# Performance work log

Hardware: AMD Instinct MI355X
Metric: run time of the kernel (lower is better)

## Reference

```python
import jax, jax.numpy as jnp
import numpy as np

N_WIN = 8
NUM_HEADS = 8
TOPK = 4
D_MODEL = 128
SCALE = D_MODEL ** (-0.5)


def setup_inputs() -> dict:
    key = jax.random.key(0)
    k1, k2 = jax.random.split(key)
    cv_feature = jax.random.normal(k1, (1, 128, 128, 128), dtype=jnp.float32)
    mv_feature = jax.random.normal(k2, (1, 2, 128, 128, 128), dtype=jnp.float32)
    return {"cv_feature": cv_feature, "mv_feature": mv_feature}


def reference(cv_feature, mv_feature):
    # cv_feature: [N, H, W, C] query view; mv_feature: [N, V, H, W, C] multi-view KV
    N, H, W, C = cv_feature.shape
    V = mv_feature.shape[1]
    j = i = N_WIN
    h, w = H // j, W // i
    p2, w2 = j * i, h * w
    ch = C // NUM_HEADS  # per-head dim

    # window partition: n (j h) (i w) c -> n (j i) h w c
    cv_patch = cv_feature.reshape(N, j, h, i, w, C).transpose(0, 1, 3, 2, 4, 5).reshape(N, p2, h, w, C)
    mv_patch = mv_feature.reshape(N, V, j, h, i, w, C).transpose(0, 1, 2, 4, 3, 5, 6).reshape(N, V, p2, h, w, C)

    q_pix = cv_patch.reshape(N, p2, w2, C)          # [N, p2, w2, C]
    kv_pix = mv_patch.reshape(N, V, p2, w2, C)      # [N, V, p2, w2, C]

    # window-level descriptors (means) -> routing logits
    q_win = cv_patch.mean(axis=(2, 3))              # [N, p2, C]
    k_win = mv_patch.mean(axis=(3, 4))              # [N, V, p2, C]

    # TopK routing (detached in original; forward math identical)
    k_flat = k_win.reshape(N, V * p2, C)
    attn_logit = jnp.einsum('npc,nqc->npq', q_win * SCALE, k_flat)  # [N, p2, V*p2]
    topk_logit, r_idx = jax.lax.top_k(attn_logit, TOPK)
    r_weight = jax.nn.softmax(topk_logit, axis=-1)  # computed by module, unused downstream

    # KV gather of selected windows: [N, p2, topk, w2, C]
    kv_flat = kv_pix.reshape(N, V * p2, w2, C)
    kv_sel = kv_flat[jnp.arange(N)[:, None, None], r_idx]

    # per-window multi-head attention over topk*w2 gathered tokens
    q = q_pix.reshape(N, p2, w2, NUM_HEADS, ch)
    kv = kv_sel.reshape(N, p2, TOPK * w2, NUM_HEADS, ch)
    attn = jnp.einsum('npwmc,npxmc->npmwx', q * SCALE, kv)  # [N, p2, m, w2, topk*w2]
    attn = jax.nn.softmax(attn, axis=-1)
    out = jnp.einsum('npmwx,npxmc->npwmc', attn, kv)        # [N, p2, w2, m, ch]

    # merge windows back: n (j i) (h w) c -> n (j h) (i w) c
    out = out.reshape(N, j, i, h, w, C).transpose(0, 1, 3, 2, 4, 5).reshape(N, H, W, C)
    return out
```

## Files before the change

### kernel.cpp

```cpp
#include <hip/hip_runtime.h>

#define HH_ 128
#define WW_ 128
#define CC_ 128
#define P2 64
#define W2 256
#define NH 8
#define CH 16
#define NV 2
#define TOPK 4
#define SCALE 0.08838834764831845f

typedef unsigned short u16;
typedef unsigned int   u32;
typedef short s8v __attribute__((ext_vector_type(8)));
typedef float f4  __attribute__((ext_vector_type(4)));

union FRAG { uint4 q; u32 u[4]; s8v v; };

__device__ float g_means[(P2 + NV * P2) * CC_];
__device__ int2  g_part[64];
__device__ int   g_mode;
__device__ int   g_amb;

__device__ inline u16 f2b(float v) {
    union { float f; u32 u; } x; x.f = v;
    u32 r = x.u + 0x7FFFu + ((x.u >> 16) & 1u);
    return (u16)(r >> 16);
}
__device__ inline float b2f(u16 h) {
    union { u32 u; float f; } x; x.u = (u32)h << 16; return x.f;
}
__device__ inline float h2f(u16 h) {
    u32 s = (h >> 15) & 1u, e = (h >> 10) & 31u, m = h & 1023u;
    float v;
    if (e == 0)       v = m * 5.9604644775e-8f;
    else if (e == 31) v = 65504.f;
    else { union { u32 u; float f; } x; x.u = ((e + 112u) << 23) | (m << 13); v = x.f; }
    return s ? -v : v;
}
__device__ inline u16 f2h(float v) {
    union { float f; u32 u; } x; x.f = v;
    u32 s = (x.u >> 16) & 0x8000u;
    int  e = (int)((x.u >> 23) & 0xFF) - 112;
    u32  m = x.u & 0x7FFFFF;
    if (e >= 31) return (u16)(s | 0x7BFF);
    if (e <= 0) {
        if (e < -10) return (u16)s;
        m |= 0x800000u;
        int sh = 14 - e;
        u32 r = m >> sh, rem = m & ((1u << sh) - 1u), half = 1u << (sh - 1);
        if (rem > half || (rem == half && (r & 1))) r++;
        return (u16)(s | r);
    }
    u32 r = ((u32)e << 10) | (m >> 13), rem = m & 0x1FFFu;
    if (rem > 0x1000u || (rem == 0x1000u && (r & 1))) r++;
    return (u16)(s | r);
}

__device__ inline u32 pkhi(float a, float b) {
    union { float f; u32 u; } xa, xb; xa.f = a; xb.f = b;
    return (xa.u >> 16) | (xb.u & 0xFFFF0000u);
}
__device__ inline float hipart(float a) {
    union { float f; u32 u; } x; x.f = a; x.u &= 0xFFFF0000u; return x.f;
}

template<int MODE>
__device__ inline float decode1(const void* __restrict__ src, int off) {
    if (MODE == 0) return ((const float*)src)[off];
    u16 h = ((const u16*)src)[off];
    return (MODE == 1) ? b2f(h) : h2f(h);
}

template<int MODE>
__device__ inline float4 loadf4(const void* __restrict__ src, int off) {
    if (MODE == 0) return *(const float4*)((const float*)src + off);
    uint2 v = *(const uint2*)((const u16*)src + off);
    float4 r;
    if (MODE == 1) {
        r.x = b2f((u16)v.x); r.y = b2f((u16)(v.x >> 16));
        r.z = b2f((u16)v.y); r.w = b2f((u16)(v.y >> 16));
    } else {
        r.x = h2f((u16)v.x); r.y = h2f((u16)(v.x >> 16));
        r.z = h2f((u16)v.y); r.w = h2f((u16)(v.y >> 16));
    }
    return r;
}

template<int MODE>
__device__ inline void store4t(void* __restrict__ out, int off, const float* __restrict__ r) {
    if (MODE == 0) {
        *(float4*)((float*)out + off) = make_float4(r[0], r[1], r[2], r[3]);
    } else if (MODE == 1) {
        u32 w0 = (u32)f2b(r[0]) | ((u32)f2b(r[1]) << 16);
        u32 w1 = (u32)f2b(r[2]) | ((u32)f2b(r[3]) << 16);
        *(uint2*)((u16*)out + off) = make_uint2(w0, w1);
    } else {
        u32 w0 = (u32)f2h(r[0]) | ((u32)f2h(r[1]) << 16);
        u32 w1 = (u32)f2h(r[2]) | ((u32)f2h(r[3]) << 16);
        *(uint2*)((u16*)out + off) = make_uint2(w0, w1);
    }
}

__global__ void detect_sample(const void* __restrict__ cv, int n) {
    __shared__ int bc[2];
    int tid = threadIdx.x, k = blockIdx.x;
    if (tid < 2) bc[tid] = 0;
    __syncthreads();
    int lim32 = n / 2;
    int lim16 = n / 2;
    u32 r = ((u32)(tid + k * 257) * 2654435761u);
    int j32 = (int)(r % (u32)lim32);
    float a = fabsf(((const float*)cv)[j32]);
    bool c0 = (a >= 1e-4f && a <= 1e4f);
    int j16 = 2 * (int)((r >> 8) % (u32)lim16);
    float b = fabsf(b2f(((const u16*)cv)[j16]));
    bool c1 = (b >= 1e-4f && b <= 1e4f);
    unsigned long long b0 = __ballot(c0);
    unsigned long long b1 = __ballot(c1);
    if ((tid & 63) == 0) {
        atomicAdd(&bc[0], __popcll(b0));
        atomicAdd(&bc[1], __popcll(b1));
    }
    __syncthreads();
    if (tid == 0) g_part[k] = make_int2(bc[0], bc[1]);
}

__global__ void detect_final() {
    int tid = threadIdx.x;
    int2 v = g_part[tid];
    int c0 = v.x, c1 = v.y;
#pragma unroll
    for (int off = 32; off >= 1; off >>= 1) {
        c0 += __shfl_down(c0, off);
        c1 += __shfl_down(c1, off);
    }
    if (tid == 0) {
        const float T = 256.f * 64.f;
        float f0 = c0 / T, f1 = c1 / T;
        int mode, amb = 0;
        if (f1 >= 0.85f) mode = 1;
        else if (f0 >= 0.80f) mode = 0;
        else mode = 2;
        if ((f1 > 0.60f && f1 < 0.85f) || (mode != 1 && f0 > 0.65f && f0 < 0.80f)) amb = 1;
        g_mode = mode; g_amb = amb;
    }
}

template<int MODE>
__device__ inline void wm_accum(const void* __restrict__ src, int voff, int jj, int ii,
                                int pc, int c0, float* __restrict__ acc) {
#pragma unroll
    for (int k = 0; k < 8; ++k) {
        int px = 8 * pc + k;
        int hh = px >> 4, ww = px & 15;
        int a = voff + ((jj * 16 + hh) * WW_ + ii * 16 + ww) * CC_ + c0;
        if (MODE == 0) {
            const float4* p4 = (const float4*)((const float*)src + a);
            float4 x = p4[0], y = p4[1];
            acc[0] += x.x; acc[1] += x.y; acc[2] += x.z; acc[3] += x.w;
            acc[4] += y.x; acc[5] += y.y; acc[6] += y.z; acc[7] += y.w;
        } else {
            uint4 v = *(const uint4*)((const u16*)src + a);
            u32 wd[4] = { v.x, v.y, v.z, v.w };
#pragma unroll
            for (int j = 0; j < 4; ++j) {
                u16 lo = (u16)(wd[j] & 0xFFFFu), hi = (u16)(wd[j] >> 16);
                acc[2 * j]     += (MODE == 1) ? b2f(lo) : h2f(lo);
                acc[2 * j + 1] += (MODE == 1) ? b2f(hi) : h2f(hi);
            }
        }
    }
}

__global__ __launch_bounds__(512) void win_mean_kernel(const void* __restrict__ cv,
                                                       const void* __restrict__ mv) {
    __shared__ float part[32][128];
    int mode = g_mode;
    int row = blockIdx.x, tid = threadIdx.x;
    int o = tid & 15, pc = tid >> 4;
    const void* src; int voff = 0; int p;
    if (row < P2) { p = row; src = cv; }
    else { int r = row - P2; voff = (r >> 6) * HH_ * WW_ * CC_; p = r & 63; src = mv; }
    int jj = p >> 3, ii = p & 7;
    int c0 = 8 * o;
    float acc[8];
#pragma unroll
    for (int j = 0; j < 8; ++j) acc[j] = 0.f;
    if (mode == 0)      wm_accum<0>(src, voff, jj, ii, pc, c0, acc);
    else if (mode == 1) wm_accum<1>(src, voff, jj, ii, pc, c0, acc);
    else                wm_accum<2>(src, voff, jj, ii, pc, c0, acc);
#pragma unroll
    for (int j = 0; j < 8; ++j) part[pc][c0 + j] = acc[j];
    __syncthreads();
    if (tid < 128) {
        float s = 0.f;
#pragma unroll
        for (int k = 0; k < 32; ++k) s += part[k][tid];
        g_means[row * CC_ + tid] = s * (1.0f / 256.0f);
    }
}

template<int MODE>
__device__ void attn_body(const void* __restrict__ cv, const void* __restrict__ mv,
                          void* __restrict__ out, int p, int m, int tid,
                          u32 (* __restrict__ kfrag)[64][4],
                          u32 (* __restrict__ vfrag)[64][4],
                          const int* __restrict__ rwin) {
    int jj = p >> 3, ii = p & 7;
    int wv = tid >> 6, l = tid & 63;
    int lg = l >> 4, lr = l & 15;

    FRAG qf1[2], qf2[2];
#pragma unroll
    for (int qi = 0; qi < 2; ++qi) {
        int qrow = wv * 32 + qi * 16 + lr;
        int hh = qrow >> 4, ww = qrow & 15;
        int pix = (jj * 16 + hh) * WW_ + (ii * 16 + ww);
        float4 qv = loadf4<MODE>(cv, pix * CC_ + m * CH + 4 * lg);
        float q0 = qv.x * SCALE, q1 = qv.y * SCALE, q2 = qv.z * SCALE, q3 = qv.w * SCALE;
        u32 h01 = pkhi(q0, q1), h23 = pkhi(q2, q3);
        u32 l01 = pkhi(q0 - hipart(q0), q1 - hipart(q1));
        u32 l23 = pkhi(q2 - hipart(q2), q3 - hipart(q3));
        qf1[qi].u[0] = h01; qf1[qi].u[1] = h23; qf1[qi].u[2] = l01; qf1[qi].u[3] = l23;
        qf2[qi].u[0] = l01; qf2[qi].u[1] = l23; qf2[qi].u[2] = h01; qf2[qi].u[3] = h23;
    }

    int ktl0 = tid >> 6;
    int kb[4], vb[4];
#pragma unroll
    for (int g = 0; g < 4; ++g) {
        int t = rwin[g]; int v = t >> 6, pp = t & 63;
        int jj2 = pp >> 3, ii2 = pp & 7;
        int wrow = (v * HH_ + jj2 * 16) * WW_ + ii2 * 16;
        kb[g] = (wrow + lr) * CC_ + m * CH + 4 * lg;
        vb[g] = (wrow + 4 * lg) * CC_ + m * CH + lr;
    }

    float4 kraw[4];
    float  vraw[4][4];

    auto loadh = [&](int h) {
#pragma unroll
        for (int i = 0; i < 4; ++i) {
            int kt = h * 32 + ktl0 + 8 * i;
            int g = kt >> 4, hh2 = kt & 15;
            kraw[i] = loadf4<MODE>(mv, kb[g] + hh2 * (WW_ * CC_));
        }
#pragma unroll
        for (int i = 0; i < 4; ++i) {
            int kt = h * 32 + ktl0 + 8 * i;
            int g = kt >> 4, hh2 = kt & 15;
            int a = vb[g] + hh2 * (WW_ * CC_);
#pragma unroll
            for (int io = 0; io < 4; ++io)
                vraw[i][io] = decode1<MODE>(mv, a + io * CC_);
        }
    };

    auto writeh = [&]() {
#pragma unroll
        for (int i = 0; i < 4; ++i) {
            int ktl = ktl0 + 8 * i;
            float4 kc = kraw[i];
            FRAG kf;
            kf.u[0] = pkhi(kc.x, kc.y);
            kf.u[1] = pkhi(kc.z, kc.w);
            kf.u[2] = pkhi(kc.x - hipart(kc.x), kc.y - hipart(kc.y));
            kf.u[3] = pkhi(kc.z - hipart(kc.z), kc.w - hipart(kc.w));
            *(uint4*)&kfrag[ktl][l][0] = kf.q;
            float v0 = vraw[i][0], v1 = vraw[i][1], v2 = vraw[i][2], v3 = vraw[i][3];
            FRAG vf;
            vf.u[0] = pkhi(v0, v1);
            vf.u[1] = pkhi(v2, v3);
            vf.u[2] = pkhi(v0 - hipart(v0), v1 - hipart(v1));
            vf.u[3] = pkhi(v2 - hipart(v2), v3 - hipart(v3));
            *(uint4*)&vfrag[ktl][l][0] = vf.q;
        }
    };

    f4 Oacc0 = {0.f, 0.f, 0.f, 0.f};
    f4 Oacc1 = {0.f, 0.f, 0.f, 0.f};
    float lp0 = 0.f, lp1 = 0.f;
    const uint4* kbase = (const uint4*)&kfrag[0][0][0];
    const uint4* vbase = (const uint4*)&vfrag[0][0][0];

    auto computeh = [&]() {
#pragma unroll 2
        for (int ktl = 0; ktl < 32; ++ktl) {
            FRAG kf, vf, vf2;
            kf.q = kbase[ktl * 64 + l];
            vf.q = vbase[ktl * 64 + l];
            vf2.u[0] = vf.u[2]; vf2.u[1] = vf.u[3];
            vf2.u[2] = vf.u[0]; vf2.u[3] = vf.u[1];
            {
                f4 sc = {0.f, 0.f, 0.f, 0.f};
                sc = __builtin_amdgcn_mfma_f32_16x16x32_bf16(kf.v, qf1[0].v, sc, 0, 0, 0);
                sc = __builtin_amdgcn_mfma_f32_16x16x32_bf16(kf.v, qf2[0].v, sc, 0, 0, 0);
                float pe0 = __expf(fminf(sc[0], 20.f));
                float pe1 = __expf(fminf(sc[1], 20.f));
                float pe2 = __expf(fminf(sc[2], 20.f));
                float pe3 = __expf(fminf(sc[3], 20.f));
                lp0 += (pe0 + pe1) + (pe2 + pe3);
                FRAG pf;
                pf.u[0] = pkhi(pe0, pe1);
                pf.u[1] = pkhi(pe2, pe3);
                pf.u[2] = pkhi(pe0 - hipart(pe0), pe1 - hipart(pe1));
                pf.u[3] = pkhi(pe2 - hipart(pe2), pe3 - hipart(pe3));
                Oacc0 = __builtin_amdgcn_mfma_f32_16x16x32_bf16(vf.v,  pf.v, Oacc0, 0, 0, 0);
                Oacc0 = __builtin_amdgcn_mfma_f32_16x16x32_bf16(vf2.v, pf.v, Oacc0, 0, 0, 0);
            }
            {
                f4 sc = {0.f, 0.f, 0.f, 0.f};
                sc = __builtin_amdgcn_mfma_f32_16x16x32_bf16(kf.v, qf1[1].v, sc, 0, 0, 0);
                sc = __builtin_amdgcn_mfma_f32_16x16x32_bf16(kf.v, qf2[1].v, sc, 0, 0, 0);
                float pe0 = __expf(fminf(sc[0], 20.f));
                float pe1 = __expf(fminf(sc[1], 20.f));
                float pe2 = __expf(fminf(sc[2], 20.f));
                float pe3 = __expf(fminf(sc[3], 20.f));
                lp1 += (pe0 + pe1) + (pe2 + pe3);
                FRAG pf;
                pf.u[0] = pkhi(pe0, pe1);
                pf.u[1] = pkhi(pe2, pe3);
                pf.u[2] = pkhi(pe0 - hipart(pe0), pe1 - hipart(pe1));
                pf.u[3] = pkhi(pe2 - hipart(pe2), pe3 - hipart(pe3));
                Oacc1 = __builtin_amdgcn_mfma_f32_16x16x32_bf16(vf.v,  pf.v, Oacc1, 0, 0, 0);
                Oacc1 = __builtin_amdgcn_mfma_f32_16x16x32_bf16(vf2.v, pf.v, Oacc1, 0, 0, 0);
            }
        }
    };

    loadh(0);
    writeh();
    __syncthreads();
    loadh(1);
    computeh();
    __syncthreads();
    writeh();
    __syncthreads();
    computeh();

#pragma unroll
    for (int qi = 0; qi < 2; ++qi) {
        float lt = (qi == 0) ? lp0 : lp1;
        lt += __shfl_xor(lt, 16);
        lt += __shfl_xor(lt, 32);
        float inv = 1.0f / fmaxf(lt, 1e-30f);
        f4 Oa = (qi == 0) ? Oacc0 : Oacc1;
        float res[4];
#pragma unroll
        for (int r = 0; r < 4; ++r)
            res[r] = fminf(fmaxf(Oa[r] * inv, -1000.f), 1000.f);
        int qrow = wv * 32 + qi * 16 + lr;
        int hh = qrow >> 4, ww = qrow & 15;
        int pix = (jj * 16 + hh) * WW_ + (ii * 16 + ww);
        store4t<MODE>(out, pix * CC_ + m * CH + 4 * lg, res);
    }
}

__global__ __launch_bounds__(512, 4) void attn_kernel(const void* __restrict__ cv,
                                                      const void* __restrict__ mv,
                                                      void* __restrict__ out) {
    __shared__ u32 kfrag[32][64][4];
    __shared__ u32 vfrag[32][64][4];
    __shared__ float slog[NV * P2];
    __shared__ int   sridx[TOPK];

    int mode = g_mode;
    int p = blockIdx.x >> 3, m = blockIdx.x & 7;
    int tid = threadIdx.x;

    {
        int t  = tid >> 2;
        int cs = (tid & 3) << 5;
        const float4* qw = (const float4*)(g_means + p * CC_ + cs);
        const float4* kw = (const float4*)(g_means + (P2 + t) * CC_ + cs);
        float a = 0.f;
#pragma unroll
        for (int i = 0; i < 8; ++i) {
            float4 qv = qw[i], kv4 = kw[i];
            a += qv.x * kv4.x + qv.y * kv4.y + qv.z * kv4.z + qv.w * kv4.w;
        }
        a += __shfl_down(a, 2, 4);
        a += __shfl_down(a, 1, 4);
        if ((tid & 3) == 0) slog[t] = a;
    }
    __syncthreads();
    if (tid == 0) {
#pragma unroll
        for (int k = 0; k < TOPK; ++k) {
            int best = 0; float bv = slog[0];
            for (int q2 = 1; q2 < NV * P2; ++q2)
                if (slog[q2] > bv) { bv = slog[q2]; best = q2; }
            sridx[k] = best;
            slog[best] = -3.0e38f;
        }
    }
    __syncthreads();

    int rwin[TOPK];
#pragma unroll
    for (int k = 0; k < TOPK; ++k) rwin[k] = sridx[k] & 127;

    if (mode == 0)      attn_body<0>(cv, mv, out, p, m, tid, kfrag, vfrag, rwin);
    else if (mode == 1) attn_body<1>(cv, mv, out, p, m, tid, kfrag, vfrag, rwin);
    else                attn_body<2>(cv, mv, out, p, m, tid, kfrag, vfrag, rwin);
}

extern "C" void kernel_launch(void* const* d_in, const int* in_sizes, int n_in,
                              void* d_out, int out_size, void* d_ws, size_t ws_size,
                              hipStream_t stream) {
    const void* cv = d_in[0];
    const void* mv = d_in[1];
    int n_cv = in_sizes[0];
    if (n_in >= 2 && in_sizes[0] > in_sizes[1]) { cv = d_in[1]; mv = d_in[0]; n_cv = in_sizes[1]; }
    (void)d_ws; (void)ws_size; (void)out_size;

    detect_sample<<<64, 256, 0, stream>>>(cv, n_cv);
    detect_final<<<1, 64, 0, stream>>>();
    win_mean_kernel<<<192, 512, 0, stream>>>(cv, mv);
    attn_kernel<<<P2 * NH, 512, 0, stream>>>(cv, mv, d_out);
}
```

Before: 142.1 us.

## Stage KV in four 16-tile chunks to halve LDS and raise occupancy; use exp2

Changes the KV staging pipeline from two 32-tile halves to four 16-tile chunks, one per selected routing window. This halves the shared memory for K/V fragments and lets launch bounds request 8 waves per EU instead of 4. It also folds log2(e) into the query scale so the softmax uses a native exp2 instead of __expf. More chunks add more __syncthreads barriers, and the tighter register budget may cause spills.

```diff
diff --git a/kernel.cpp b/kernel.cpp
--- a/kernel.cpp
+++ b/kernel.cpp
@@ -10,11 +10,19 @@
 #define NV 2
 #define TOPK 4
 #define SCALE 0.08838834764831845f
+#define SCALE_L2E 0.1275216f
+#define CLAMP_L2 28.8539f
 
 typedef unsigned short u16;
 typedef unsigned int   u32;
 typedef short s8v __attribute__((ext_vector_type(8)));
 typedef float f4  __attribute__((ext_vector_type(4)));
+
+#if __has_builtin(__builtin_amdgcn_exp2f)
+#define EXP2(x) __builtin_amdgcn_exp2f(x)
+#else
+#define EXP2(x) exp2f(x)
+#endif
 
 union FRAG { uint4 q; u32 u[4]; s8v v; };
 
@@ -219,7 +227,8 @@
         int hh = qrow >> 4, ww = qrow & 15;
         int pix = (jj * 16 + hh) * WW_ + (ii * 16 + ww);
         float4 qv = loadf4<MODE>(cv, pix * CC_ + m * CH + 4 * lg);
-        float q0 = qv.x * SCALE, q1 = qv.y * SCALE, q2 = qv.z * SCALE, q3 = qv.w * SCALE;
+        float q0 = qv.x * SCALE_L2E, q1 = qv.y * SCALE_L2E;
+        float q2 = qv.z * SCALE_L2E, q3 = qv.w * SCALE_L2E;
         u32 h01 = pkhi(q0, q1), h23 = pkhi(q2, q3);
         u32 l01 = pkhi(q0 - hipart(q0), q1 - hipart(q1));
         u32 l23 = pkhi(q2 - hipart(q2), q3 - hipart(q3));
@@ -228,31 +237,24 @@
     }
 
     int ktl0 = tid >> 6;
-    int kb[4], vb[4];
-#pragma unroll
-    for (int g = 0; g < 4; ++g) {
-        int t = rwin[g]; int v = t >> 6, pp = t & 63;
+    float4 kraw[2];
+    float  vraw[2][4];
+
+    auto loadh = [&](int r) {
+        int t = rwin[r]; int v = t >> 6, pp = t & 63;
         int jj2 = pp >> 3, ii2 = pp & 7;
         int wrow = (v * HH_ + jj2 * 16) * WW_ + ii2 * 16;
-        kb[g] = (wrow + lr) * CC_ + m * CH + 4 * lg;
-        vb[g] = (wrow + 4 * lg) * CC_ + m * CH + lr;
-    }
-
-    float4 kraw[4];
-    float  vraw[4][4];
-
-    auto loadh = [&](int h) {
-#pragma unroll
-        for (int i = 0; i < 4; ++i) {
-            int kt = h * 32 + ktl0 + 8 * i;
-            int g = kt >> 4, hh2 = kt & 15;
-            kraw[i] = loadf4<MODE>(mv, kb[g] + hh2 * (WW_ * CC_));
-        }
-#pragma unroll
-        for (int i = 0; i < 4; ++i) {
-            int kt = h * 32 + ktl0 + 8 * i;
-            int g = kt >> 4, hh2 = kt & 15;
-            int a = vb[g] + hh2 * (WW_ * CC_);
+        int kbr = (wrow + lr) * CC_ + m * CH + 4 * lg;
+        int vbr = (wrow + 4 * lg) * CC_ + m * CH + lr;
+#pragma unroll
+        for (int i = 0; i < 2; ++i) {
+            int ktl = ktl0 + 8 * i;
+            kraw[i] = loadf4<MODE>(mv, kbr + ktl * (WW_ * CC_));
+        }
+#pragma unroll
+        for (int i = 0; i < 2; ++i) {
+            int ktl = ktl0 + 8 * i;
+            int a = vbr + ktl * (WW_ * CC_);
 #pragma unroll
             for (int io = 0; io < 4; ++io)
                 vraw[i][io] = decode1<MODE>(mv, a + io * CC_);
@@ -261,7 +263,7 @@
 
     auto writeh = [&]() {
 #pragma unroll
-        for (int i = 0; i < 4; ++i) {
+        for (int i = 0; i < 2; ++i) {
             int ktl = ktl0 + 8 * i;
             float4 kc = kraw[i];
             FRAG kf;
@@ -283,25 +285,25 @@
     f4 Oacc0 = {0.f, 0.f, 0.f, 0.f};
     f4 Oacc1 = {0.f, 0.f, 0.f, 0.f};
     float lp0 = 0.f, lp1 = 0.f;
-    const uint4* kbase = (const uint4*)&kfrag[0][0][0];
-    const uint4* vbase = (const uint4*)&vfrag[0][0][0];
+    const uint4* kp = (const uint4*)&kfrag[0][0][0] + l;
+    const uint4* vp = (const uint4*)&vfrag[0][0][0] + l;
 
     auto computeh = [&]() {
-#pragma unroll 2
-        for (int ktl = 0; ktl < 32; ++ktl) {
+#pragma unroll 4
+        for (int ktl = 0; ktl < 16; ++ktl) {
             FRAG kf, vf, vf2;
-            kf.q = kbase[ktl * 64 + l];
-            vf.q = vbase[ktl * 64 + l];
+            kf.q = kp[ktl * 64];
+            vf.q = vp[ktl * 64];
             vf2.u[0] = vf.u[2]; vf2.u[1] = vf.u[3];
             vf2.u[2] = vf.u[0]; vf2.u[3] = vf.u[1];
             {
                 f4 sc = {0.f, 0.f, 0.f, 0.f};
                 sc = __builtin_amdgcn_mfma_f32_16x16x32_bf16(kf.v, qf1[0].v, sc, 0, 0, 0);
                 sc = __builtin_amdgcn_mfma_f32_16x16x32_bf16(kf.v, qf2[0].v, sc, 0, 0, 0);
-                float pe0 = __expf(fminf(sc[0], 20.f));
-                float pe1 = __expf(fminf(sc[1], 20.f));
-                float pe2 = __expf(fminf(sc[2], 20.f));
-                float pe3 = __expf(fminf(sc[3], 20.f));
+                float pe0 = EXP2(fminf(sc[0], CLAMP_L2));
+                float pe1 = EXP2(fminf(sc[1], CLAMP_L2));
+                float pe2 = EXP2(fminf(sc[2], CLAMP_L2));
+                float pe3 = EXP2(fminf(sc[3], CLAMP_L2));
                 lp0 += (pe0 + pe1) + (pe2 + pe3);
                 FRAG pf;
                 pf.u[0] = pkhi(pe0, pe1);
@@ -315,10 +317,10 @@
                 f4 sc = {0.f, 0.f, 0.f, 0.f};
                 sc = __builtin_amdgcn_mfma_f32_16x16x32_bf16(kf.v, qf1[1].v, sc, 0, 0, 0);
                 sc = __builtin_amdgcn_mfma_f32_16x16x32_bf16(kf.v, qf2[1].v, sc, 0, 0, 0);
-                float pe0 = __expf(fminf(sc[0], 20.f));
-                float pe1 = __expf(fminf(sc[1], 20.f));
-                float pe2 = __expf(fminf(sc[2], 20.f));
-                float pe3 = __expf(fminf(sc[3], 20.f));
+                float pe0 = EXP2(fminf(sc[0], CLAMP_L2));
+                float pe1 = EXP2(fminf(sc[1], CLAMP_L2));
+                float pe2 = EXP2(fminf(sc[2], CLAMP_L2));
+                float pe3 = EXP2(fminf(sc[3], CLAMP_L2));
                 lp1 += (pe0 + pe1) + (pe2 + pe3);
                 FRAG pf;
                 pf.u[0] = pkhi(pe0, pe1);
@@ -334,11 +336,14 @@
     loadh(0);
     writeh();
     __syncthreads();
-    loadh(1);
-    computeh();
-    __syncthreads();
-    writeh();
-    __syncthreads();
+#pragma unroll 1
+    for (int r = 1; r < 4; ++r) {
+        loadh(r);
+        computeh();
+        __syncthreads();
+        writeh();
+        __syncthreads();
+    }
     computeh();
 
 #pragma unroll
@@ -359,11 +364,11 @@
     }
 }
 
-__global__ __launch_bounds__(512, 4) void attn_kernel(const void* __restrict__ cv,
+__global__ __launch_bounds__(512, 8) void attn_kernel(const void* __restrict__ cv,
                                                       const void* __restrict__ mv,
                                                       void* __restrict__ out) {
-    __shared__ u32 kfrag[32][64][4];
-    __shared__ u32 vfrag[32][64][4];
+    __shared__ u32 kfrag[16][64][4];
+    __shared__ u32 vfrag[16][64][4];
     __shared__ float slog[NV * P2];
     __shared__ int   sridx[TOPK];
 
```

Result: slower. 150.3 us (+5.8%).
